# Kernel optimization log

Hardware: AMD Instinct MI355X
Metric: run time of the kernel (lower is better)

Reference implementation:

```python
import jax, jax.numpy as jnp
import numpy as np

HEADS = 24
HEAD_DIM = 128
COND = 1024      # (512//8)*(512//8)*16//64
TXTLEN = 128
EPS = 1e-6


def setup_inputs() -> dict:
    key = jax.random.key(0)
    ks = jax.random.split(key, 16)
    S, D, R = 2176, 3072, 16
    f = lambda k, shp, s=1.0: jax.random.normal(k, shp, dtype=jnp.float32) * s
    return {
        "hidden_states": f(ks[0], (1, S, D)),
        "Wq": f(ks[1], (D, D), 0.02), "bq": f(ks[2], (D,), 0.02),
        "Wk": f(ks[3], (D, D), 0.02), "bk": f(ks[4], (D,), 0.02),
        "Wv": f(ks[5], (D, D), 0.02), "bv": f(ks[6], (D,), 0.02),
        "q_down": f(ks[7], (R, D), 1.0 / R), "q_up": f(ks[8], (D, R), 0.02),
        "k_down": f(ks[9], (R, D), 1.0 / R), "k_up": f(ks[10], (D, R), 0.02),
        "v_down": f(ks[11], (R, D), 1.0 / R), "v_up": f(ks[12], (D, R), 0.02),
        "norm_q_w": jnp.ones((HEAD_DIM,), jnp.float32),
        "norm_k_w": jnp.ones((HEAD_DIM,), jnp.float32),
        "rope_cos": f(ks[13], (S, HEAD_DIM)),
        "rope_sin": f(ks[14], (S, HEAD_DIM)),
    }


def _rms_norm(x, w):
    # per-head RMSNorm over head_dim
    var = jnp.mean(x * x, axis=-1, keepdims=True)
    return x * jax.lax.rsqrt(var + EPS) * w


def _apply_rope(x, cos, sin):
    # diffusers apply_rotary_emb, use_real=True, unbind_dim=-1 (interleaved pairs)
    xr = x.reshape(*x.shape[:-1], HEAD_DIM // 2, 2)
    x_rot = jnp.stack([-xr[..., 1], xr[..., 0]], axis=-1).reshape(x.shape)
    return x * cos[None, None] + x_rot * sin[None, None]


def _forward(hidden_states, Wq, bq, Wk, bk, Wv, bv,
             q_down, q_up, k_down, k_up, v_down, v_up,
             norm_q_w, norm_k_w, rope_cos, rope_sin):
    B, S, D = hidden_states.shape
    block = S - COND  # scaled_block_size

    # dense QKV projections
    q = hidden_states @ Wq.T + bq
    k = hidden_states @ Wk.T + bk
    v = hidden_states @ Wv.T + bv

    # LoRA on cond segment only (mask zeros all rows outside [block, block+COND))
    pos = jnp.arange(S)
    seg = ((pos >= block) & (pos < block + COND)).astype(hidden_states.dtype)[None, :, None]
    hm = hidden_states * seg
    # lora_weight=1.0, network_alpha/rank = 16/16 = 1.0
    q = q + (hm @ q_down.T) @ q_up.T
    k = k + (hm @ k_down.T) @ k_up.T
    v = v + (hm @ v_down.T) @ v_up.T

    # [B, H, S, hd]
    to_heads = lambda t: t.reshape(B, S, HEADS, HEAD_DIM).transpose(0, 2, 1, 3)
    q, k, v = to_heads(q), to_heads(k), to_heads(v)

    q = _rms_norm(q, norm_q_w)
    k = _rms_norm(k, norm_k_w)

    q = _apply_rope(q, rope_cos, rope_sin)
    k = _apply_rope(k, rope_cos, rope_sin)

    # additive mask: rows < block attend everything; cond rows (n_loras=1)
    # attend only their own cond block
    row, col = pos[:, None], pos[None, :]
    allowed = (row < block) | ((row >= block) & (col >= block))
    bias = jnp.where(allowed, 0.0, -1e20).astype(q.dtype)

    scale = 1.0 / np.sqrt(HEAD_DIM)
    scores = jnp.einsum("bhqd,bhkd->bhqk", q, k) * scale + bias
    attn = jax.nn.softmax(scores, axis=-1)
    out = jnp.einsum("bhqk,bhkd->bhqd", attn, v)

    out = out.transpose(0, 2, 1, 3).reshape(B, S, HEADS * HEAD_DIM)
    return out[:, :block, :]  # hidden_states (use_cond=False)


def reference(hidden_states, Wq, bq, Wk, bk, Wv, bv,
              q_down, q_up, k_down, k_up, v_down, v_up,
              norm_q_w, norm_k_w, rope_cos, rope_sin):
    return _forward(hidden_states, Wq, bq, Wk, bk, Wv, bv,
                    q_down, q_up, k_down, k_up, v_down, v_up,
                    norm_q_w, norm_k_w, rope_cos, rope_sin)
```

## Files before the change

### kernel.cpp

```cpp
#include <hip/hip_runtime.h>
#include <stdint.h>

#define Sq   2176
#define Dm   3072
#define NDm  9216
#define NH   24
#define HDm  128
#define BLKR 1152
#define KVH  1088
#define NT2  34

typedef __attribute__((ext_vector_type(8))) __bf16 bf16x8;
typedef __attribute__((ext_vector_type(4))) float f32x4;
typedef __attribute__((ext_vector_type(8))) unsigned short ushort8;

#define AS1 __attribute__((address_space(1)))
#define AS3 __attribute__((address_space(3)))

__device__ __forceinline__ unsigned short f2bf(float x) {
  unsigned u = __builtin_bit_cast(unsigned, x);
  u += 0x7FFFu + ((u >> 16) & 1u);
  return (unsigned short)(u >> 16);
}

__global__ void cvt_kernel(const float* __restrict__ src,
                           unsigned short* __restrict__ dst, int n8) {
  int i = blockIdx.x * blockDim.x + threadIdx.x;
  if (i >= n8) return;
  const float4* s4 = (const float4*)src + (size_t)i * 2;
  float4 a = s4[0], b = s4[1];
  ushort8 o;
  o[0]=f2bf(a.x); o[1]=f2bf(a.y); o[2]=f2bf(a.z); o[3]=f2bf(a.w);
  o[4]=f2bf(b.x); o[5]=f2bf(b.y); o[6]=f2bf(b.z); o[7]=f2bf(b.w);
  *((ushort8*)dst + i) = o;
}

__global__ void cvt3_kernel(const float* __restrict__ w0, const float* __restrict__ w1,
                            const float* __restrict__ w2,
                            unsigned short* __restrict__ dst, int n8) {
  int i = blockIdx.x * blockDim.x + threadIdx.x;
  if (i >= n8) return;
  const float* src = blockIdx.y == 0 ? w0 : (blockIdx.y == 1 ? w1 : w2);
  const float4* s4 = (const float4*)src + (size_t)i * 2;
  float4 a = s4[0], b = s4[1];
  ushort8 o;
  o[0]=f2bf(a.x); o[1]=f2bf(a.y); o[2]=f2bf(a.z); o[3]=f2bf(a.w);
  o[4]=f2bf(b.x); o[5]=f2bf(b.y); o[6]=f2bf(b.z); o[7]=f2bf(b.w);
  *((ushort8*)dst + (size_t)blockIdx.y * (Dm * (size_t)Dm / 8) + i) = o;
}

__global__ __launch_bounds__(256, 4) void gemm_kernel(
    const unsigned short* __restrict__ A,
    const unsigned short* __restrict__ B,
    const float* __restrict__ bq, const float* __restrict__ bk,
    const float* __restrict__ bv, float* __restrict__ C) {
  __shared__ __attribute__((aligned(16))) unsigned short aL[128 * 64];
  __shared__ __attribute__((aligned(16))) unsigned short bL[128 * 64];
  int t = threadIdx.x;
  int wid = t >> 6, lane = t & 63;
  int lr = lane & 15, lg = lane >> 4;
  int wr = wid >> 1, wc = wid & 1;

  int bid = blockIdx.x;
  int wg = (bid & 7) * 129 + (bid >> 3);
  int mt, nt;
  if (wg < 216) { nt = wg / 9; mt = wg % 9; }
  else { int r2 = wg - 216; nt = 24 + r2 / 17; mt = r2 % 17; }
  int m0 = mt * 128, n0 = nt * 128;

  f32x4 acc[4][4];
#pragma unroll
  for (int m = 0; m < 4; m++)
#pragma unroll
    for (int n = 0; n < 4; n++) acc[m][n] = (f32x4){0.f, 0.f, 0.f, 0.f};

  int tr = t >> 3;
  int uu = (t & 7) ^ (tr & 7);
  const unsigned short* pA = A + (size_t)(m0 + tr) * Dm + uu * 8;
  const unsigned short* pB = B + (size_t)(n0 + tr) * Dm + uu * 8;

  int lr7 = lr & 7;
  int baseA = (wr * 64 + lr) * 64;
  int baseB = (wc * 64 + lr) * 64;
  int d0 = (lg ^ lr7) * 8;
  int d1 = ((4 + lg) ^ lr7) * 8;

  for (int kt = 0; kt < Dm / 64; kt++) {
    const int ko = kt * 64;
#pragma unroll
    for (int c = 0; c < 4; c++) {
      __builtin_amdgcn_global_load_lds(
          (const AS1 void*)(pA + (size_t)c * 32 * Dm + ko),
          (AS3 void*)(&aL[c * 2048 + wid * 512]), 16, 0, 0);
      __builtin_amdgcn_global_load_lds(
          (const AS1 void*)(pB + (size_t)c * 32 * Dm + ko),
          (AS3 void*)(&bL[c * 2048 + wid * 512]), 16, 0, 0);
    }
    __syncthreads();

    bf16x8 a0[4], b0[4];
#pragma unroll
    for (int m = 0; m < 4; m++) a0[m] = *(const bf16x8*)&aL[baseA + m * 1024 + d0];
#pragma unroll
    for (int n = 0; n < 4; n++) b0[n] = *(const bf16x8*)&bL[baseB + n * 1024 + d0];
#pragma unroll
    for (int m = 0; m < 4; m++)
#pragma unroll
      for (int n = 0; n < 4; n++)
        acc[m][n] = __builtin_amdgcn_mfma_f32_16x16x32_bf16(a0[m], b0[n], acc[m][n], 0, 0, 0);

    bf16x8 a1[4], b1[4];
#pragma unroll
    for (int m = 0; m < 4; m++) a1[m] = *(const bf16x8*)&aL[baseA + m * 1024 + d1];
#pragma unroll
    for (int n = 0; n < 4; n++) b1[n] = *(const bf16x8*)&bL[baseB + n * 1024 + d1];
#pragma unroll
    for (int m = 0; m < 4; m++)
#pragma unroll
      for (int n = 0; n < 4; n++)
        acc[m][n] = __builtin_amdgcn_mfma_f32_16x16x32_bf16(a1[m], b1[n], acc[m][n], 0, 0, 0);
    __syncthreads();
  }

#pragma unroll
  for (int m = 0; m < 4; m++)
#pragma unroll
    for (int n = 0; n < 4; n++) {
      int col = n0 + wc * 64 + n * 16 + lr;
      float bias = col < 3072 ? bq[col] : (col < 6144 ? bk[col - 3072] : bv[col - 6144]);
#pragma unroll
      for (int i = 0; i < 4; i++) {
        int r = m0 + wr * 64 + m * 16 + lg * 4 + i;
        C[(size_t)r * NDm + col] = acc[m][n][i] + bias;
      }
    }
}

__global__ __launch_bounds__(256) void lora_kernel(
    const float* __restrict__ hs,
    const float* __restrict__ k_down, const float* __restrict__ k_up,
    const float* __restrict__ v_down, const float* __restrict__ v_up,
    float* __restrict__ qkv) {
  int srow = BLKR + blockIdx.x;
  int t = threadIdx.x;
  __shared__ float hsl[Dm];
  __shared__ float tl[32];
  for (int e = t; e < Dm; e += 256) hsl[e] = hs[(size_t)srow * Dm + e];
  __syncthreads();
  int dot = t >> 3, part = t & 7;
  int mat = dot >> 4, j = dot & 15;
  const float* down = mat ? v_down : k_down;
  float p = 0.f;
  for (int e = part; e < Dm; e += 8) p += hsl[e] * down[j * Dm + e];
  p += __shfl_xor(p, 1, 64);
  p += __shfl_xor(p, 2, 64);
  p += __shfl_xor(p, 4, 64);
  if (part == 0) tl[dot] = p;
  __syncthreads();
  float tk[16], tv[16];
#pragma unroll
  for (int jj = 0; jj < 16; jj++) { tk[jj] = tl[jj]; tv[jj] = tl[16 + jj]; }
  for (int n = t; n < Dm; n += 256) {
    float ak = 0.f, av = 0.f;
#pragma unroll
    for (int jj = 0; jj < 16; jj++) {
      ak += tk[jj] * k_up[n * 16 + jj];
      av += tv[jj] * v_up[n * 16 + jj];
    }
    qkv[(size_t)srow * NDm + 3072 + n] += ak;
    qkv[(size_t)srow * NDm + 6144 + n] += av;
  }
}

__global__ __launch_bounds__(256) void prep_kernel(
    const float* __restrict__ qkv,
    const float* __restrict__ nqw, const float* __restrict__ nkw,
    const float* __restrict__ rc, const float* __restrict__ rs,
    unsigned short* __restrict__ qh, unsigned short* __restrict__ kh) {
  int s = blockIdx.x;
  int w = threadIdx.x >> 6, l = threadIdx.x & 63;
  int d0 = l * 2;
  float c0 = rc[s * 128 + d0], c1 = rc[s * 128 + d0 + 1];
  float s0 = rs[s * 128 + d0], s1 = rs[s * 128 + d0 + 1];
  float wk0 = nkw[d0], wk1 = nkw[d0 + 1];
  float wq0 = nqw[d0], wq1 = nqw[d0 + 1];
  bool doq = (s < BLKR);

#pragma unroll
  for (int hh = 0; hh < 6; hh++) {
    int h = w * 6 + hh;
    {
      const float* kp = qkv + (size_t)s * NDm + 3072 + h * 128;
      float2 x = *(const float2*)(kp + d0);
      float ss = x.x * x.x + x.y * x.y;
#pragma unroll
      for (int m = 1; m < 64; m <<= 1) ss += __shfl_xor(ss, m, 64);
      float r = rsqrtf(ss * (1.f / 128.f) + 1e-6f);
      float xn0 = x.x * r * wk0, xn1 = x.y * r * wk1;
      ushort2 o = make_ushort2(f2bf(xn0 * c0 - xn1 * s0), f2bf(xn1 * c1 + xn0 * s1));
      *(ushort2*)&kh[((size_t)h * Sq + s) * 128 + d0] = o;
    }
    if (doq) {
      const float* qp = qkv + (size_t)s * NDm + h * 128;
      float2 x = *(const float2*)(qp + d0);
      float ss = x.x * x.x + x.y * x.y;
#pragma unroll
      for (int m = 1; m < 64; m <<= 1) ss += __shfl_xor(ss, m, 64);
      float r = rsqrtf(ss * (1.f / 128.f) + 1e-6f);
      float xn0 = x.x * r * wq0, xn1 = x.y * r * wq1;
      ushort2 o = make_ushort2(f2bf(xn0 * c0 - xn1 * s0), f2bf(xn1 * c1 + xn0 * s1));
      *(ushort2*)&qh[((size_t)h * BLKR + s) * 128 + d0] = o;
    }
  }
}

__global__ __launch_bounds__(256) void vt_kernel(const float* __restrict__ qkv,
                                                 unsigned short* __restrict__ vt) {
  int st = blockIdx.x, dt = blockIdx.y, h = blockIdx.z;
  int tx = threadIdx.x & 31, ty = threadIdx.x >> 5;
  __shared__ float ld[32][33];
  int s0 = st * 32, d0 = dt * 32;
#pragma unroll
  for (int p = 0; p < 4; p++) {
    int ss = ty + p * 8;
    ld[ss][tx] = qkv[(size_t)(s0 + ss) * NDm + 6144 + h * 128 + d0 + tx];
  }
  __syncthreads();
#pragma unroll
  for (int p = 0; p < 4; p++) {
    int dd = ty + p * 8;
    vt[((size_t)h * 128 + d0 + dd) * Sq + s0 + tx] = f2bf(ld[tx][dd]);
  }
}

__global__ __launch_bounds__(256) void attn_kernel(
    const unsigned short* __restrict__ qh,
    const unsigned short* __restrict__ kh,
    const unsigned short* __restrict__ vt,
    float* __restrict__ accW,
    float* __restrict__ lW) {
  int bid = blockIdx.x;
  int wg = (bid & 7) * 108 + (bid >> 3);
  int h = wg / 36, rem = wg % 36;
  int qt = rem >> 1, split = rem & 1;
  int q0 = qt * 64;
  int k0 = split * KVH;

  int t = threadIdx.x;
  int w = t >> 6, lane = t & 63;
  int lr = lane & 15, lg = lane >> 4;

  __shared__ __attribute__((aligned(16))) unsigned short kLds[2][32 * 128];
  __shared__ __attribute__((aligned(16))) unsigned short vLds[2][128 * 32];

  const unsigned short* qb = qh + ((size_t)h * BLKR + q0 + w * 16) * 128;
  bf16x8 aq[4];
#pragma unroll
  for (int m = 0; m < 4; m++)
    aq[m] = *(const bf16x8*)(qb + (size_t)lr * 128 + m * 32 + lg * 8);

  const unsigned short* kh_h = kh + ((size_t)h * Sq + k0) * 128;
  const unsigned short* vt_h = vt + (size_t)h * 128 * Sq + k0;

  const unsigned short* srcK[2];
  const unsigned short* srcV[2];
  int kDst[2], vDst[2];
#pragma unroll
  for (int c = 0; c < 2; c++) {
    int u = c * 256 + t;
    int rK = u >> 4, sK = u & 15;
    srcK[c] = kh_h + (size_t)rK * 128 + ((sK ^ (rK & 7)) * 8);
    kDst[c] = u * 8;
    int rV = u >> 2, sV = u & 3;
    srcV[c] = vt_h + (size_t)rV * Sq + ((sV ^ (rV & 3)) * 8);
    vDst[c] = u * 8;
  }

  auto stage = [&](int kt, int buf) {
#pragma unroll
    for (int c = 0; c < 2; c++)
      __builtin_amdgcn_global_load_lds(
          (const AS1 void*)(srcK[c] + (size_t)kt * 4096),
          (AS3 void*)(&kLds[buf][kDst[c]]), 16, 0, 0);
#pragma unroll
    for (int c = 0; c < 2; c++)
      __builtin_amdgcn_global_load_lds(
          (const AS1 void*)(srcV[c] + (size_t)kt * 32),
          (AS3 void*)(&vLds[buf][vDst[c]]), 16, 0, 0);
  };

  f32x4 acc[8];
#pragma unroll
  for (int o = 0; o < 8; o++) acc[o] = (f32x4){0.f, 0.f, 0.f, 0.f};
  float lsum = 0.f;
  const float sc = 0.08838834764831845f;
  const float L2E = 1.4426950408889634f;
  const float ea = sc * L2E, eb = -10.0f * L2E;

  int lr7 = lr & 7, lr3 = lr & 3;
  int adLo = ((((lg & 1) << 1)) * 16 + lr) * 4;
  int adHi = adLo + 64;
  bool hiKb = (lg & 2) != 0;

  auto compute = [&](int buf) {
    const unsigned short* kbuf = kLds[buf];
    const unsigned short* vbuf = vLds[buf];
    f32x4 s2[2];
    s2[0] = (f32x4){0.f, 0.f, 0.f, 0.f};
    s2[1] = (f32x4){0.f, 0.f, 0.f, 0.f};
    __builtin_amdgcn_s_setprio(1);
#pragma unroll
    for (int kb = 0; kb < 2; kb++)
#pragma unroll
      for (int m = 0; m < 4; m++) {
        bf16x8 kf = *(const bf16x8*)&kbuf[(kb * 16 + lr) * 128 + ((m * 4 + lg) ^ lr7) * 8];
        s2[kb] = __builtin_amdgcn_mfma_f32_16x16x32_bf16(kf, aq[m], s2[kb], 0, 0, 0);
      }
    __builtin_amdgcn_s_setprio(0);
    unsigned pk0[2], pk1[2];
#pragma unroll
    for (int kb = 0; kb < 2; kb++) {
      float p0 = exp2f(fmaf(s2[kb][0], ea, eb));
      float p1 = exp2f(fmaf(s2[kb][1], ea, eb));
      float p2 = exp2f(fmaf(s2[kb][2], ea, eb));
      float p3 = exp2f(fmaf(s2[kb][3], ea, eb));
      lsum += (p0 + p1) + (p2 + p3);
      unsigned r0, r1;
      asm("v_cvt_pk_bf16_f32 %0, %1, %2" : "=v"(r0) : "v"(p0), "v"(p1));
      asm("v_cvt_pk_bf16_f32 %0, %1, %2" : "=v"(r1) : "v"(p2), "v"(p3));
      if (kb == 0) { pk0[0] = r0; pk0[1] = r1; }
      else         { pk1[0] = r0; pk1[1] = r1; }
    }
    int a00 = __builtin_amdgcn_ds_bpermute(adLo, (int)pk0[0]);
    int a01 = __builtin_amdgcn_ds_bpermute(adLo, (int)pk0[1]);
    int a10 = __builtin_amdgcn_ds_bpermute(adLo, (int)pk1[0]);
    int a11 = __builtin_amdgcn_ds_bpermute(adLo, (int)pk1[1]);
    int b00 = __builtin_amdgcn_ds_bpermute(adHi, (int)pk0[0]);
    int b01 = __builtin_amdgcn_ds_bpermute(adHi, (int)pk0[1]);
    int b10 = __builtin_amdgcn_ds_bpermute(adHi, (int)pk1[0]);
    int b11 = __builtin_amdgcn_ds_bpermute(adHi, (int)pk1[1]);
    int4 pw;
    pw.x = hiKb ? a10 : a00;
    pw.y = hiKb ? a11 : a01;
    pw.z = hiKb ? b10 : b00;
    pw.w = hiKb ? b11 : b01;
    bf16x8 pfrag = __builtin_bit_cast(bf16x8, pw);
    __builtin_amdgcn_s_setprio(1);
#pragma unroll
    for (int o = 0; o < 8; o++) {
      bf16x8 vf = *(const bf16x8*)&vbuf[(o * 16 + lr) * 32 + (lg ^ lr3) * 8];
      acc[o] = __builtin_amdgcn_mfma_f32_16x16x32_bf16(vf, pfrag, acc[o], 0, 0, 0);
    }
    __builtin_amdgcn_s_setprio(0);
  };

  stage(0, 0);
  __syncthreads();
  for (int kt = 0; kt < NT2; kt += 2) {
    stage(kt + 1, 1);
    compute(0);
    __syncthreads();
    if (kt + 2 < NT2) stage(kt + 2, 0);
    compute(1);
    __syncthreads();
  }

  lsum += __shfl_xor(lsum, 16, 64);
  lsum += __shfl_xor(lsum, 32, 64);

  float* accP = accW + (size_t)split * BLKR * 3072;
  size_t rowOff = (size_t)(q0 + w * 16 + lr) * 3072 + h * 128;
#pragma unroll
  for (int o = 0; o < 8; o++)
    *(f32x4*)&accP[rowOff + o * 16 + lg * 4] = acc[o];
  if (lg == 0) {
    float* lP = lW + (size_t)split * NH * BLKR + (size_t)h * BLKR;
    lP[q0 + w * 16 + lr] = lsum;
  }
}

__global__ __launch_bounds__(256) void normalize_kernel(
    const float* __restrict__ accW, const float* __restrict__ lW,
    float* __restrict__ out) {
  int idx = blockIdx.x * 256 + threadIdx.x;
  int r = idx / 384, rem = idx % 384;
  int c = rem * 8, h = c >> 7;
  const float4* a0 = (const float4*)(accW + (size_t)r * 3072 + c);
  const float4* a1 = (const float4*)(accW + (size_t)BLKR * 3072 + (size_t)r * 3072 + c);
  float l = lW[(size_t)h * BLKR + r] + lW[(size_t)NH * BLKR + (size_t)h * BLKR + r];
  float inv = 1.0f / l;
  float4 v0 = a0[0], v1 = a0[1], u0 = a1[0], u1 = a1[1];
  float4 o0, o1;
  o0.x = (v0.x + u0.x) * inv; o0.y = (v0.y + u0.y) * inv;
  o0.z = (v0.z + u0.z) * inv; o0.w = (v0.w + u0.w) * inv;
  o1.x = (v1.x + u1.x) * inv; o1.y = (v1.y + u1.y) * inv;
  o1.z = (v1.z + u1.z) * inv; o1.w = (v1.w + u1.w) * inv;
  float4* op = (float4*)(out + (size_t)r * 3072 + c);
  op[0] = o0; op[1] = o1;
}

extern "C" void kernel_launch(void* const* d_in, const int* in_sizes, int n_in,
                              void* d_out, int out_size, void* d_ws, size_t ws_size,
                              hipStream_t stream) {
  const float* hs  = (const float*)d_in[0];
  const float* Wq  = (const float*)d_in[1];
  const float* bq  = (const float*)d_in[2];
  const float* Wk  = (const float*)d_in[3];
  const float* bk  = (const float*)d_in[4];
  const float* Wv  = (const float*)d_in[5];
  const float* bv  = (const float*)d_in[6];
  const float* k_down = (const float*)d_in[9];
  const float* k_up   = (const float*)d_in[10];
  const float* v_down = (const float*)d_in[11];
  const float* v_up   = (const float*)d_in[12];
  const float* nqw = (const float*)d_in[13];
  const float* nkw = (const float*)d_in[14];
  const float* rc  = (const float*)d_in[15];
  const float* rsn = (const float*)d_in[16];
  float* out = (float*)d_out;

  char* ws = (char*)d_ws;
  unsigned short* hsb = (unsigned short*)(ws + 0);
  unsigned short* wb  = (unsigned short*)(ws + 13369344);
  float*          qkv = (float*)(ws + 69992448);
  unsigned short* qh  = (unsigned short*)(ws + 150208512);
  unsigned short* kh  = (unsigned short*)(ws + 157286400);
  unsigned short* vtb = (unsigned short*)(ws + 170655744);
  float* accW = qkv;
  float* lW   = (float*)(ws + 69992448 + 28311552);

  const int n8_hs = Sq * Dm / 8;
  const int n8_w  = Dm * Dm / 8;
  cvt_kernel<<<dim3((n8_hs + 255) / 256), 256, 0, stream>>>(hs, hsb, n8_hs);
  cvt3_kernel<<<dim3((n8_w + 255) / 256, 3), 256, 0, stream>>>(Wq, Wk, Wv, wb, n8_w);

  gemm_kernel<<<dim3(1032), 256, 0, stream>>>(hsb, wb, bq, bk, bv, qkv);
  lora_kernel<<<dim3(Sq - BLKR), 256, 0, stream>>>(hs, k_down, k_up, v_down, v_up, qkv);
  prep_kernel<<<dim3(Sq), 256, 0, stream>>>(qkv, nqw, nkw, rc, rsn, qh, kh);
  vt_kernel<<<dim3(Sq / 32, HDm / 32, NH), 256, 0, stream>>>(qkv, vtb);
  attn_kernel<<<dim3(2 * 18 * NH), 256, 0, stream>>>(qh, kh, vtb, accW, lW);
  normalize_kernel<<<dim3(BLKR * 3072 / 8 / 256), 256, 0, stream>>>(accW, lW, out);
}
```

Before: 363.1 us.

## Fuse LoRA up-projection, RMSNorm, RoPE and V transpose into the QKV GEMM epilogue

The LoRA down-projection now runs as a small pre-pass that writes only the rank-16 intermediates. The QKV GEMM epilogue then adds the LoRA up-projection as one extra MFMA step through shared memory, computes per-head RMSNorm with cross-wave reductions, applies RoPE, and writes bf16 Q/K heads and transposed V directly. This removes the fp32 QKV round trip through global memory and the separate lora, prep and vt kernel launches. In exchange the epilogue is heavier, uses more registers and shared memory, and the LoRA contribution is now computed in bf16, which costs some precision.

```diff
diff --git a/kernel.cpp b/kernel.cpp
--- a/kernel.cpp
+++ b/kernel.cpp
@@ -49,98 +49,10 @@
   *((ushort8*)dst + (size_t)blockIdx.y * (Dm * (size_t)Dm / 8) + i) = o;
 }
 
-__global__ __launch_bounds__(256, 4) void gemm_kernel(
-    const unsigned short* __restrict__ A,
-    const unsigned short* __restrict__ B,
-    const float* __restrict__ bq, const float* __restrict__ bk,
-    const float* __restrict__ bv, float* __restrict__ C) {
-  __shared__ __attribute__((aligned(16))) unsigned short aL[128 * 64];
-  __shared__ __attribute__((aligned(16))) unsigned short bL[128 * 64];
-  int t = threadIdx.x;
-  int wid = t >> 6, lane = t & 63;
-  int lr = lane & 15, lg = lane >> 4;
-  int wr = wid >> 1, wc = wid & 1;
-
-  int bid = blockIdx.x;
-  int wg = (bid & 7) * 129 + (bid >> 3);
-  int mt, nt;
-  if (wg < 216) { nt = wg / 9; mt = wg % 9; }
-  else { int r2 = wg - 216; nt = 24 + r2 / 17; mt = r2 % 17; }
-  int m0 = mt * 128, n0 = nt * 128;
-
-  f32x4 acc[4][4];
-#pragma unroll
-  for (int m = 0; m < 4; m++)
-#pragma unroll
-    for (int n = 0; n < 4; n++) acc[m][n] = (f32x4){0.f, 0.f, 0.f, 0.f};
-
-  int tr = t >> 3;
-  int uu = (t & 7) ^ (tr & 7);
-  const unsigned short* pA = A + (size_t)(m0 + tr) * Dm + uu * 8;
-  const unsigned short* pB = B + (size_t)(n0 + tr) * Dm + uu * 8;
-
-  int lr7 = lr & 7;
-  int baseA = (wr * 64 + lr) * 64;
-  int baseB = (wc * 64 + lr) * 64;
-  int d0 = (lg ^ lr7) * 8;
-  int d1 = ((4 + lg) ^ lr7) * 8;
-
-  for (int kt = 0; kt < Dm / 64; kt++) {
-    const int ko = kt * 64;
-#pragma unroll
-    for (int c = 0; c < 4; c++) {
-      __builtin_amdgcn_global_load_lds(
-          (const AS1 void*)(pA + (size_t)c * 32 * Dm + ko),
-          (AS3 void*)(&aL[c * 2048 + wid * 512]), 16, 0, 0);
-      __builtin_amdgcn_global_load_lds(
-          (const AS1 void*)(pB + (size_t)c * 32 * Dm + ko),
-          (AS3 void*)(&bL[c * 2048 + wid * 512]), 16, 0, 0);
-    }
-    __syncthreads();
-
-    bf16x8 a0[4], b0[4];
-#pragma unroll
-    for (int m = 0; m < 4; m++) a0[m] = *(const bf16x8*)&aL[baseA + m * 1024 + d0];
-#pragma unroll
-    for (int n = 0; n < 4; n++) b0[n] = *(const bf16x8*)&bL[baseB + n * 1024 + d0];
-#pragma unroll
-    for (int m = 0; m < 4; m++)
-#pragma unroll
-      for (int n = 0; n < 4; n++)
-        acc[m][n] = __builtin_amdgcn_mfma_f32_16x16x32_bf16(a0[m], b0[n], acc[m][n], 0, 0, 0);
-
-    bf16x8 a1[4], b1[4];
-#pragma unroll
-    for (int m = 0; m < 4; m++) a1[m] = *(const bf16x8*)&aL[baseA + m * 1024 + d1];
-#pragma unroll
-    for (int n = 0; n < 4; n++) b1[n] = *(const bf16x8*)&bL[baseB + n * 1024 + d1];
-#pragma unroll
-    for (int m = 0; m < 4; m++)
-#pragma unroll
-      for (int n = 0; n < 4; n++)
-        acc[m][n] = __builtin_amdgcn_mfma_f32_16x16x32_bf16(a1[m], b1[n], acc[m][n], 0, 0, 0);
-    __syncthreads();
-  }
-
-#pragma unroll
-  for (int m = 0; m < 4; m++)
-#pragma unroll
-    for (int n = 0; n < 4; n++) {
-      int col = n0 + wc * 64 + n * 16 + lr;
-      float bias = col < 3072 ? bq[col] : (col < 6144 ? bk[col - 3072] : bv[col - 6144]);
-#pragma unroll
-      for (int i = 0; i < 4; i++) {
-        int r = m0 + wr * 64 + m * 16 + lg * 4 + i;
-        C[(size_t)r * NDm + col] = acc[m][n][i] + bias;
-      }
-    }
-}
-
-__global__ __launch_bounds__(256) void lora_kernel(
+__global__ __launch_bounds__(256) void lorat_kernel(
     const float* __restrict__ hs,
-    const float* __restrict__ k_down, const float* __restrict__ k_up,
-    const float* __restrict__ v_down, const float* __restrict__ v_up,
-    float* __restrict__ qkv) {
+    const float* __restrict__ k_down, const float* __restrict__ v_down,
+    float* __restrict__ tkW, float* __restrict__ tvW) {
   int srow = BLKR + blockIdx.x;
   int t = threadIdx.x;
   __shared__ float hsl[Dm];
@@ -157,79 +69,191 @@
   p += __shfl_xor(p, 4, 64);
   if (part == 0) tl[dot] = p;
   __syncthreads();
-  float tk[16], tv[16];
-#pragma unroll
-  for (int jj = 0; jj < 16; jj++) { tk[jj] = tl[jj]; tv[jj] = tl[16 + jj]; }
-  for (int n = t; n < Dm; n += 256) {
-    float ak = 0.f, av = 0.f;
-#pragma unroll
-    for (int jj = 0; jj < 16; jj++) {
-      ak += tk[jj] * k_up[n * 16 + jj];
-      av += tv[jj] * v_up[n * 16 + jj];
-    }
-    qkv[(size_t)srow * NDm + 3072 + n] += ak;
-    qkv[(size_t)srow * NDm + 6144 + n] += av;
-  }
-}
-
-__global__ __launch_bounds__(256) void prep_kernel(
-    const float* __restrict__ qkv,
+  if (t < 16) tkW[(size_t)blockIdx.x * 16 + t] = tl[t];
+  else if (t < 32) tvW[(size_t)blockIdx.x * 16 + (t - 16)] = tl[t];
+}
+
+__global__ __launch_bounds__(256, 4) void gemm_kernel(
+    const unsigned short* __restrict__ A,
+    const unsigned short* __restrict__ B,
+    const float* __restrict__ bq, const float* __restrict__ bk,
+    const float* __restrict__ bv,
+    const float* __restrict__ tkW, const float* __restrict__ tvW,
+    const float* __restrict__ kup, const float* __restrict__ vup,
     const float* __restrict__ nqw, const float* __restrict__ nkw,
     const float* __restrict__ rc, const float* __restrict__ rs,
-    unsigned short* __restrict__ qh, unsigned short* __restrict__ kh) {
-  int s = blockIdx.x;
-  int w = threadIdx.x >> 6, l = threadIdx.x & 63;
-  int d0 = l * 2;
-  float c0 = rc[s * 128 + d0], c1 = rc[s * 128 + d0 + 1];
-  float s0 = rs[s * 128 + d0], s1 = rs[s * 128 + d0 + 1];
-  float wk0 = nkw[d0], wk1 = nkw[d0 + 1];
-  float wq0 = nqw[d0], wq1 = nqw[d0 + 1];
-  bool doq = (s < BLKR);
-
-#pragma unroll
-  for (int hh = 0; hh < 6; hh++) {
-    int h = w * 6 + hh;
-    {
-      const float* kp = qkv + (size_t)s * NDm + 3072 + h * 128;
-      float2 x = *(const float2*)(kp + d0);
-      float ss = x.x * x.x + x.y * x.y;
-#pragma unroll
-      for (int m = 1; m < 64; m <<= 1) ss += __shfl_xor(ss, m, 64);
-      float r = rsqrtf(ss * (1.f / 128.f) + 1e-6f);
-      float xn0 = x.x * r * wk0, xn1 = x.y * r * wk1;
-      ushort2 o = make_ushort2(f2bf(xn0 * c0 - xn1 * s0), f2bf(xn1 * c1 + xn0 * s1));
-      *(ushort2*)&kh[((size_t)h * Sq + s) * 128 + d0] = o;
+    unsigned short* __restrict__ qh, unsigned short* __restrict__ kh,
+    unsigned short* __restrict__ vtb) {
+  __shared__ __attribute__((aligned(16))) unsigned short sm[17408];
+  __shared__ float rsum[2][2][64];
+  int t = threadIdx.x;
+  int wid = t >> 6, lane = t & 63;
+  int lr = lane & 15, lg = lane >> 4;
+  int wr = wid >> 1, wc = wid & 1;
+
+  int bid = blockIdx.x;
+  int wg = (bid & 7) * 129 + (bid >> 3);
+  int mt, nt;
+  if (wg < 216) { nt = wg / 9; mt = wg % 9; }
+  else { int r2 = wg - 216; nt = 24 + r2 / 17; mt = r2 % 17; }
+  int m0 = mt * 128, n0 = nt * 128;
+
+  f32x4 acc[4][4];
+#pragma unroll
+  for (int m = 0; m < 4; m++)
+#pragma unroll
+    for (int n = 0; n < 4; n++) acc[m][n] = (f32x4){0.f, 0.f, 0.f, 0.f};
+
+  int tr = t >> 3;
+  int uu = (t & 7) ^ (tr & 7);
+  const unsigned short* pA = A + (size_t)(m0 + tr) * Dm + uu * 8;
+  const unsigned short* pB = B + (size_t)(n0 + tr) * Dm + uu * 8;
+
+  int lr7 = lr & 7;
+  int baseA = (wr * 64 + lr) * 64;
+  int baseB = (wc * 64 + lr) * 64;
+  int d0 = (lg ^ lr7) * 8;
+  int d1 = ((4 + lg) ^ lr7) * 8;
+
+  for (int kt = 0; kt < Dm / 64; kt++) {
+    const int ko = kt * 64;
+#pragma unroll
+    for (int c = 0; c < 4; c++) {
+      __builtin_amdgcn_global_load_lds(
+          (const AS1 void*)(pA + (size_t)c * 32 * Dm + ko),
+          (AS3 void*)(&sm[c * 2048 + wid * 512]), 16, 0, 0);
+      __builtin_amdgcn_global_load_lds(
+          (const AS1 void*)(pB + (size_t)c * 32 * Dm + ko),
+          (AS3 void*)(&sm[8192 + c * 2048 + wid * 512]), 16, 0, 0);
     }
-    if (doq) {
-      const float* qp = qkv + (size_t)s * NDm + h * 128;
-      float2 x = *(const float2*)(qp + d0);
-      float ss = x.x * x.x + x.y * x.y;
-#pragma unroll
-      for (int m = 1; m < 64; m <<= 1) ss += __shfl_xor(ss, m, 64);
-      float r = rsqrtf(ss * (1.f / 128.f) + 1e-6f);
-      float xn0 = x.x * r * wq0, xn1 = x.y * r * wq1;
-      ushort2 o = make_ushort2(f2bf(xn0 * c0 - xn1 * s0), f2bf(xn1 * c1 + xn0 * s1));
-      *(ushort2*)&qh[((size_t)h * BLKR + s) * 128 + d0] = o;
+    __syncthreads();
+
+    bf16x8 a0[4], b0[4];
+#pragma unroll
+    for (int m = 0; m < 4; m++) a0[m] = *(const bf16x8*)&sm[baseA + m * 1024 + d0];
+#pragma unroll
+    for (int n = 0; n < 4; n++) b0[n] = *(const bf16x8*)&sm[8192 + baseB + n * 1024 + d0];
+#pragma unroll
+    for (int m = 0; m < 4; m++)
+#pragma unroll
+      for (int n = 0; n < 4; n++)
+        acc[m][n] = __builtin_amdgcn_mfma_f32_16x16x32_bf16(a0[m], b0[n], acc[m][n], 0, 0, 0);
+
+    bf16x8 a1[4], b1[4];
+#pragma unroll
+    for (int m = 0; m < 4; m++) a1[m] = *(const bf16x8*)&sm[baseA + m * 1024 + d1];
+#pragma unroll
+    for (int n = 0; n < 4; n++) b1[n] = *(const bf16x8*)&sm[8192 + baseB + n * 1024 + d1];
+#pragma unroll
+    for (int m = 0; m < 4; m++)
+#pragma unroll
+      for (int n = 0; n < 4; n++)
+        acc[m][n] = __builtin_amdgcn_mfma_f32_16x16x32_bf16(a1[m], b1[n], acc[m][n], 0, 0, 0);
+    __syncthreads();
+  }
+
+  int region = nt < 24 ? 0 : (nt < 48 ? 1 : 2);
+  int h = region == 0 ? nt : (region == 1 ? nt - 24 : nt - 48);
+  int dcol[4];
+#pragma unroll
+  for (int n = 0; n < 4; n++) dcol[n] = wc * 64 + n * 16 + lr;
+  const float* bias = region == 0 ? bq : (region == 1 ? bk : bv);
+#pragma unroll
+  for (int n = 0; n < 4; n++) {
+    float b = bias[h * 128 + dcol[n]];
+#pragma unroll
+    for (int m = 0; m < 4; m++)
+#pragma unroll
+      for (int i = 0; i < 4; i++) acc[m][n][i] += b;
+  }
+
+  if (region >= 1 && m0 >= BLKR) {
+    const float* tW = region == 1 ? tkW : tvW;
+    const float* up = region == 1 ? kup : vup;
+    int rr = t >> 1, half = t & 1;
+    const float* srcT = tW + ((size_t)(m0 - BLKR) + rr) * 16 + half * 8;
+    const float* srcU = up + ((size_t)h * 128 + rr) * 16 + half * 8;
+    ushort8 vT, vU;
+#pragma unroll
+    for (int u2 = 0; u2 < 8; u2++) { vT[u2] = f2bf(srcT[u2]); vU[u2] = f2bf(srcU[u2]); }
+    ushort8 z = {0, 0, 0, 0, 0, 0, 0, 0};
+    *(ushort8*)&sm[(rr * 8 + (half ^ (rr & 7))) * 8] = vT;
+    *(ushort8*)&sm[(rr * 8 + ((2 + half) ^ (rr & 7))) * 8] = z;
+    *(ushort8*)&sm[8192 + (rr * 8 + (half ^ (rr & 7))) * 8] = vU;
+    *(ushort8*)&sm[8192 + (rr * 8 + ((2 + half) ^ (rr & 7))) * 8] = z;
+    __syncthreads();
+    bf16x8 a0[4], b0[4];
+#pragma unroll
+    for (int m = 0; m < 4; m++) a0[m] = *(const bf16x8*)&sm[baseA + m * 1024 + d0];
+#pragma unroll
+    for (int n = 0; n < 4; n++) b0[n] = *(const bf16x8*)&sm[8192 + baseB + n * 1024 + d0];
+#pragma unroll
+    for (int m = 0; m < 4; m++)
+#pragma unroll
+      for (int n = 0; n < 4; n++)
+        acc[m][n] = __builtin_amdgcn_mfma_f32_16x16x32_bf16(a0[m], b0[n], acc[m][n], 0, 0, 0);
+    __syncthreads();
+  }
+
+  if (region <= 1) {
+    float part[4][4];
+#pragma unroll
+    for (int m = 0; m < 4; m++)
+#pragma unroll
+      for (int i = 0; i < 4; i++) {
+        float p = acc[m][0][i] * acc[m][0][i] + acc[m][1][i] * acc[m][1][i]
+                + acc[m][2][i] * acc[m][2][i] + acc[m][3][i] * acc[m][3][i];
+#pragma unroll
+        for (int d = 1; d < 16; d <<= 1) p += __shfl_xor(p, d, 64);
+        part[m][i] = p;
+      }
+    if (lr == 0) {
+#pragma unroll
+      for (int m = 0; m < 4; m++)
+#pragma unroll
+        for (int i = 0; i < 4; i++) rsum[wr][wc][m * 16 + lg * 4 + i] = part[m][i];
     }
-  }
-}
-
-__global__ __launch_bounds__(256) void vt_kernel(const float* __restrict__ qkv,
-                                                 unsigned short* __restrict__ vt) {
-  int st = blockIdx.x, dt = blockIdx.y, h = blockIdx.z;
-  int tx = threadIdx.x & 31, ty = threadIdx.x >> 5;
-  __shared__ float ld[32][33];
-  int s0 = st * 32, d0 = dt * 32;
-#pragma unroll
-  for (int p = 0; p < 4; p++) {
-    int ss = ty + p * 8;
-    ld[ss][tx] = qkv[(size_t)(s0 + ss) * NDm + 6144 + h * 128 + d0 + tx];
-  }
-  __syncthreads();
-#pragma unroll
-  for (int p = 0; p < 4; p++) {
-    int dd = ty + p * 8;
-    vt[((size_t)h * 128 + d0 + dd) * Sq + s0 + tx] = f2bf(ld[tx][dd]);
+    __syncthreads();
+    const float* nw = region == 0 ? nqw : nkw;
+    float wv[4];
+#pragma unroll
+    for (int n = 0; n < 4; n++) wv[n] = nw[dcol[n]];
+    unsigned short* dstb = region == 0 ? qh : kh;
+    int srows = region == 0 ? BLKR : Sq;
+#pragma unroll
+    for (int m = 0; m < 4; m++)
+#pragma unroll
+      for (int i = 0; i < 4; i++) {
+        int idx = m * 16 + lg * 4 + i;
+        float s2 = rsum[wr][0][idx] + rsum[wr][1][idx];
+        float rinv = rsqrtf(s2 * (1.f / 128.f) + 1e-6f);
+        int r = m0 + wr * 64 + idx;
+#pragma unroll
+        for (int n = 0; n < 4; n++) {
+          float xn = acc[m][n][i] * rinv * wv[n];
+          float xp = __shfl_xor(xn, 1, 64);
+          float c = rc[r * 128 + dcol[n]];
+          float s = rs[r * 128 + dcol[n]];
+          float rot = (dcol[n] & 1) ? xp : -xp;
+          dstb[((size_t)h * srows + r) * 128 + dcol[n]] = f2bf(xn * c + rot * s);
+        }
+      }
+  } else {
+#pragma unroll
+    for (int m = 0; m < 4; m++)
+#pragma unroll
+      for (int i = 0; i < 4; i++) {
+        int rl = wr * 64 + m * 16 + lg * 4 + i;
+#pragma unroll
+        for (int n = 0; n < 4; n++)
+          sm[dcol[n] * 136 + rl] = f2bf(acc[m][n][i]);
+      }
+    __syncthreads();
+    int d = t >> 1, rc0 = (t & 1) * 64;
+    unsigned short* dv = vtb + ((size_t)h * 128 + d) * Sq + m0 + rc0;
+#pragma unroll
+    for (int u = 0; u < 8; u++)
+      *(ushort8*)(dv + u * 8) = *(const ushort8*)&sm[d * 136 + rc0 + u * 8];
   }
 }
 
@@ -422,22 +446,23 @@
   char* ws = (char*)d_ws;
   unsigned short* hsb = (unsigned short*)(ws + 0);
   unsigned short* wb  = (unsigned short*)(ws + 13369344);
-  float*          qkv = (float*)(ws + 69992448);
+  float* accW = (float*)(ws + 69992448);
+  float* lW   = (float*)(ws + 98304000);
+  float* tkW  = (float*)(ws + 98525184);
+  float* tvW  = (float*)(ws + 98590720);
   unsigned short* qh  = (unsigned short*)(ws + 150208512);
   unsigned short* kh  = (unsigned short*)(ws + 157286400);
   unsigned short* vtb = (unsigned short*)(ws + 170655744);
-  float* accW = qkv;
-  float* lW   = (float*)(ws + 69992448 + 28311552);
 
   const int n8_hs = Sq * Dm / 8;
   const int n8_w  = Dm * Dm / 8;
   cvt_kernel<<<dim3((n8_hs + 255) / 256), 256, 0, stream>>>(hs, hsb, n8_hs);
   cvt3_kernel<<<dim3((n8_w + 255) / 256, 3), 256, 0, stream>>>(Wq, Wk, Wv, wb, n8_w);
-
-  gemm_kernel<<<dim3(1032), 256, 0, stream>>>(hsb, wb, bq, bk, bv, qkv);
-  lora_kernel<<<dim3(Sq - BLKR), 256, 0, stream>>>(hs, k_down, k_up, v_down, v_up, qkv);
-  prep_kernel<<<dim3(Sq), 256, 0, stream>>>(qkv, nqw, nkw, rc, rsn, qh, kh);
-  vt_kernel<<<dim3(Sq / 32, HDm / 32, NH), 256, 0, stream>>>(qkv, vtb);
+  lorat_kernel<<<dim3(Sq - BLKR), 256, 0, stream>>>(hs, k_down, v_down, tkW, tvW);
+
+  gemm_kernel<<<dim3(1032), 256, 0, stream>>>(hsb, wb, bq, bk, bv,
+                                              tkW, tvW, k_up, v_up,
+                                              nqw, nkw, rc, rsn, qh, kh, vtb);
   attn_kernel<<<dim3(2 * 18 * NH), 256, 0, stream>>>(qh, kh, vtb, accW, lW);
   normalize_kernel<<<dim3(BLKR * 3072 / 8 / 256), 256, 0, stream>>>(accW, lW, out);
 }
```

Result: faster. 304.0 us (-16.3%).
